# Kernel optimization log

Hardware: AMD Instinct MI355X
Metric: run time of the kernel (lower is better)

The kernel has to match this reference:

```python
import jax, jax.numpy as jnp
import numpy as np

N = 8192
K = 64

def setup_inputs() -> dict:
    key = jax.random.key(0)
    kw, ky = jax.random.split(key)
    W = jax.random.uniform(kw, (N, N), dtype=jnp.float32)
    Y = jax.random.normal(ky, (N, K), dtype=jnp.float32)
    return {"W": W, "Y": Y}

def reference(W, Y):
    # SpectralNetLoss(normalized=False):
    #   Dy[i,j] = ||y_i - y_j||^2 ; loss = sum(W * Dy) / (2n)
    n = Y.shape[0]
    sq = jnp.sum(Y * Y, axis=1)                      # (n,)
    # squared pairwise distances: ||y_i||^2 + ||y_j||^2 - 2 y_i.y_j
    Dy = sq[:, None] + sq[None, :] - 2.0 * (Y @ Y.T)  # (n, n)
    Dy = jnp.maximum(Dy, 0.0)  # clamp tiny negatives from cancellation (cdist is nonneg)
    loss = jnp.sum(W * Dy) / (2.0 * n)
    return loss
```

## Files before the change

### kernel.cpp

```cpp
#include <hip/hip_runtime.h>
#include <stdint.h>

#define N 8192
#define K 64
#define TILE 128
#define JT 8
#define NSTEP (4 * JT)

typedef __attribute__((ext_vector_type(8))) short bf16x8;
typedef __attribute__((ext_vector_type(4))) float floatx4;
typedef __attribute__((ext_vector_type(4))) unsigned short ushort4v;

__global__ __launch_bounds__(256) void prep_kernel(const float* __restrict__ Y,
                                                   unsigned short* __restrict__ Ybf,
                                                   float* __restrict__ sq,
                                                   float* __restrict__ out) {
    if (blockIdx.x == 0 && threadIdx.x == 0) out[0] = 0.0f;
    const int t = blockIdx.x * 256 + threadIdx.x;
    floatx4 v = *reinterpret_cast<const floatx4*>(Y + (size_t)t * 4);
    ushort4v o;
    #pragma unroll
    for (int e = 0; e < 4; ++e) {
        uint32_t bits = __float_as_uint(v[e]);
        uint32_t rnd  = bits + 0x7FFF + ((bits >> 16) & 1);
        o[e] = (unsigned short)(rnd >> 16);
    }
    *reinterpret_cast<ushort4v*>(Ybf + (size_t)t * 4) = o;
    float s = v[0]*v[0] + v[1]*v[1] + v[2]*v[2] + v[3]*v[3];
    #pragma unroll
    for (int m = 8; m >= 1; m >>= 1) s += __shfl_xor(s, m, 64);
    if ((threadIdx.x & 15) == 0) sq[t >> 4] = s;
}

__global__ __launch_bounds__(256, 2) void loss_kernel(const float* __restrict__ W,
                                                      const unsigned short* __restrict__ Ybf,
                                                      const float* __restrict__ sq,
                                                      float* __restrict__ out) {
    __shared__ float wsum[4];

    const int i0   = (blockIdx.x >> 3) * TILE;
    const int j0   = (blockIdx.x & 7) * (TILE * JT);
    const int tid  = threadIdx.x;
    const int wv   = tid >> 6;
    const int lane = tid & 63;
    const int qRow = (wv >> 1) * 64;
    const int qCol = (wv & 1) * 64;
    const int laneM = lane & 15;
    const int kq    = lane >> 4;

    bf16x8 afrag[2][4];
    float  sqi[4];
    #pragma unroll
    for (int mt = 0; mt < 4; ++mt) {
        const int row = i0 + qRow + mt * 16 + laneM;
        afrag[0][mt] = *reinterpret_cast<const bf16x8*>(Ybf + (size_t)row * K + kq * 8);
        afrag[1][mt] = *reinterpret_cast<const bf16x8*>(Ybf + (size_t)row * K + 32 + kq * 8);
        sqi[mt] = sq[row];
    }

    bf16x8  bfr[2][2][4];
    floatx4 sqjb[2][4];
    #pragma unroll
    for (int nt = 0; nt < 4; ++nt) {
        const int row = j0 + qCol + nt * 16 + laneM;
        bfr[0][0][nt] = *reinterpret_cast<const bf16x8*>(Ybf + (size_t)row * K + kq * 8);
        bfr[0][1][nt] = *reinterpret_cast<const bf16x8*>(Ybf + (size_t)row * K + 32 + kq * 8);
        sqjb[0][nt]   = *reinterpret_cast<const floatx4*>(sq + j0 + qCol + nt * 16 + kq * 4);
    }

    const float* wl = W + (size_t)(i0 + qRow + laneM) * N + (j0 + qCol + kq * 4);

    floatx4 wfb[4][4];
    #pragma unroll
    for (int g = 0; g < 4; ++g)
        #pragma unroll
        for (int nt = 0; nt < 4; ++nt)
            wfb[g][nt] = *reinterpret_cast<const floatx4*>(wl + (size_t)g * 16 * N + nt * 16);

    float p0 = 0.f, p1 = 0.f, p2 = 0.f, p3 = 0.f;

    #pragma unroll
    for (int s = 0; s < NSTEP; ++s) {
        const int mt  = s & 3;
        const int jt  = s >> 2;
        const int buf = jt & 1;

        if (mt == 0 && jt + 1 < JT) {
            #pragma unroll
            for (int nt = 0; nt < 4; ++nt) {
                const int row = j0 + (jt + 1) * TILE + qCol + nt * 16 + laneM;
                bfr[buf ^ 1][0][nt] = *reinterpret_cast<const bf16x8*>(Ybf + (size_t)row * K + kq * 8);
                bfr[buf ^ 1][1][nt] = *reinterpret_cast<const bf16x8*>(Ybf + (size_t)row * K + 32 + kq * 8);
                sqjb[buf ^ 1][nt]   = *reinterpret_cast<const floatx4*>(sq + j0 + (jt + 1) * TILE + qCol + nt * 16 + kq * 4);
            }
        }

        floatx4 accv[4];
        #pragma unroll
        for (int nt = 0; nt < 4; ++nt) accv[nt] = (floatx4){0.f, 0.f, 0.f, 0.f};
        #pragma unroll
        for (int ks = 0; ks < 2; ++ks)
            #pragma unroll
            for (int nt = 0; nt < 4; ++nt)
                accv[nt] = __builtin_amdgcn_mfma_f32_16x16x32_bf16(bfr[buf][ks][nt], afrag[ks][mt], accv[nt], 0, 0, 0);

        const float si = sqi[mt];
        #pragma unroll
        for (int nt = 0; nt < 4; ++nt) {
            const floatx4 g  = accv[nt];
            const floatx4 w4 = wfb[s & 3][nt];
            const floatx4 sj = sqjb[buf][nt];
            p0 = fmaf(w4[0], fmaxf(si + sj[0] - 2.0f * g[0], 0.f), p0);
            p1 = fmaf(w4[1], fmaxf(si + sj[1] - 2.0f * g[1], 0.f), p1);
            p2 = fmaf(w4[2], fmaxf(si + sj[2] - 2.0f * g[2], 0.f), p2);
            p3 = fmaf(w4[3], fmaxf(si + sj[3] - 2.0f * g[3], 0.f), p3);
        }

        if (s + 4 < NSTEP) {
            #pragma unroll
            for (int nt = 0; nt < 4; ++nt)
                wfb[s & 3][nt] = *reinterpret_cast<const floatx4*>(
                    wl + (size_t)mt * 16 * N + (jt + 1) * TILE + nt * 16);
        }
    }

    float partial = (p0 + p1) + (p2 + p3);
    #pragma unroll
    for (int m = 32; m >= 1; m >>= 1) partial += __shfl_xor(partial, m, 64);
    if (lane == 0) wsum[wv] = partial;
    __syncthreads();
    if (tid == 0) {
        float tot = (wsum[0] + wsum[1]) + (wsum[2] + wsum[3]);
        atomicAdd(out, tot * (1.0f / (2.0f * (float)N)));
    }
}

extern "C" void kernel_launch(void* const* d_in, const int* in_sizes, int n_in,
                              void* d_out, int out_size, void* d_ws, size_t ws_size,
                              hipStream_t stream) {
    const float* W = (const float*)d_in[0];
    const float* Y = (const float*)d_in[1];
    float* out = (float*)d_out;

    unsigned short* Ybf = (unsigned short*)d_ws;
    float* sq = (float*)((char*)d_ws + (size_t)N * K * 2);

    prep_kernel<<<(N * K / 4) / 256, 256, 0, stream>>>(Y, Ybf, sq, out);
    loss_kernel<<<(N / TILE) * (N / (TILE * JT)), 256, 0, stream>>>(W, Ybf, sq, out);
}
```

Before: 376.8 us.

## Shrink per-wave tiles and quadruple grid for higher occupancy

Reorganizes the loss kernel so each wave handles 32 rows by 256 columns instead of a 64x64 quadrant swept over 8 tiles. The grid grows from 512 to 2048 blocks, with launch bounds raised to 4 blocks per CU. W is double-buffered per 32-column step, and B fragments are loaded directly each iteration. The aim is more memory-level parallelism and lower register pressure for streaming W, at the cost of a shallower per-wave prefetch and repeated Y fragment loads.

```diff
diff --git a/kernel.cpp b/kernel.cpp
--- a/kernel.cpp
+++ b/kernel.cpp
@@ -3,9 +3,7 @@
 
 #define N 8192
 #define K 64
-#define TILE 128
-#define JT 8
-#define NSTEP (4 * JT)
+#define JT_PER 8
 
 typedef __attribute__((ext_vector_type(8))) short bf16x8;
 typedef __attribute__((ext_vector_type(4))) float floatx4;
@@ -32,95 +30,93 @@
     if ((threadIdx.x & 15) == 0) sq[t >> 4] = s;
 }
 
-__global__ __launch_bounds__(256, 2) void loss_kernel(const float* __restrict__ W,
+__global__ __launch_bounds__(256, 4) void loss_kernel(const float* __restrict__ W,
                                                       const unsigned short* __restrict__ Ybf,
                                                       const float* __restrict__ sq,
                                                       float* __restrict__ out) {
     __shared__ float wsum[4];
 
-    const int i0   = (blockIdx.x >> 3) * TILE;
-    const int j0   = (blockIdx.x & 7) * (TILE * JT);
+    const int bid  = blockIdx.x;
+    const int i0   = (bid >> 5) * 128;
+    const int j0   = (bid & 31) * 256;
     const int tid  = threadIdx.x;
     const int wv   = tid >> 6;
     const int lane = tid & 63;
-    const int qRow = (wv >> 1) * 64;
-    const int qCol = (wv & 1) * 64;
     const int laneM = lane & 15;
     const int kq    = lane >> 4;
+    const int iw    = i0 + wv * 32;
 
-    bf16x8 afrag[2][4];
-    float  sqi[4];
+    bf16x8 a[2][2];
+    float  sqi[2];
     #pragma unroll
-    for (int mt = 0; mt < 4; ++mt) {
-        const int row = i0 + qRow + mt * 16 + laneM;
-        afrag[0][mt] = *reinterpret_cast<const bf16x8*>(Ybf + (size_t)row * K + kq * 8);
-        afrag[1][mt] = *reinterpret_cast<const bf16x8*>(Ybf + (size_t)row * K + 32 + kq * 8);
-        sqi[mt] = sq[row];
+    for (int mt = 0; mt < 2; ++mt) {
+        const int row = iw + mt * 16 + laneM;
+        a[mt][0] = *reinterpret_cast<const bf16x8*>(Ybf + (size_t)row * K + kq * 8);
+        a[mt][1] = *reinterpret_cast<const bf16x8*>(Ybf + (size_t)row * K + 32 + kq * 8);
+        sqi[mt]  = sq[row];
     }
 
-    bf16x8  bfr[2][2][4];
-    floatx4 sqjb[2][4];
+    const float* wp0 = W + (size_t)(iw + laneM) * N + j0 + kq * 4;
+    const float* wp1 = wp0 + (size_t)16 * N;
+
+    floatx4 wbuf[2][2][2];
     #pragma unroll
-    for (int nt = 0; nt < 4; ++nt) {
-        const int row = j0 + qCol + nt * 16 + laneM;
-        bfr[0][0][nt] = *reinterpret_cast<const bf16x8*>(Ybf + (size_t)row * K + kq * 8);
-        bfr[0][1][nt] = *reinterpret_cast<const bf16x8*>(Ybf + (size_t)row * K + 32 + kq * 8);
-        sqjb[0][nt]   = *reinterpret_cast<const floatx4*>(sq + j0 + qCol + nt * 16 + kq * 4);
+    for (int nt = 0; nt < 2; ++nt) {
+        wbuf[0][0][nt] = *reinterpret_cast<const floatx4*>(wp0 + nt * 16);
+        wbuf[0][1][nt] = *reinterpret_cast<const floatx4*>(wp1 + nt * 16);
     }
-
-    const float* wl = W + (size_t)(i0 + qRow + laneM) * N + (j0 + qCol + kq * 4);
-
-    floatx4 wfb[4][4];
-    #pragma unroll
-    for (int g = 0; g < 4; ++g)
-        #pragma unroll
-        for (int nt = 0; nt < 4; ++nt)
-            wfb[g][nt] = *reinterpret_cast<const floatx4*>(wl + (size_t)g * 16 * N + nt * 16);
 
     float p0 = 0.f, p1 = 0.f, p2 = 0.f, p3 = 0.f;
 
     #pragma unroll
-    for (int s = 0; s < NSTEP; ++s) {
-        const int mt  = s & 3;
-        const int jt  = s >> 2;
-        const int buf = jt & 1;
+    for (int jt = 0; jt < JT_PER; ++jt) {
+        const int pp = jt & 1;
+        const int jb = j0 + jt * 32;
 
-        if (mt == 0 && jt + 1 < JT) {
+        bf16x8  b[2][2];
+        floatx4 sjq[2];
+        #pragma unroll
+        for (int nt = 0; nt < 2; ++nt) {
+            const int rowj = jb + nt * 16 + laneM;
+            b[nt][0] = *reinterpret_cast<const bf16x8*>(Ybf + (size_t)rowj * K + kq * 8);
+            b[nt][1] = *reinterpret_cast<const bf16x8*>(Ybf + (size_t)rowj * K + 32 + kq * 8);
+            sjq[nt]  = *reinterpret_cast<const floatx4*>(sq + jb + nt * 16 + kq * 4);
+        }
+
+        if (jt + 1 < JT_PER) {
             #pragma unroll
-            for (int nt = 0; nt < 4; ++nt) {
-                const int row = j0 + (jt + 1) * TILE + qCol + nt * 16 + laneM;
-                bfr[buf ^ 1][0][nt] = *reinterpret_cast<const bf16x8*>(Ybf + (size_t)row * K + kq * 8);
-                bfr[buf ^ 1][1][nt] = *reinterpret_cast<const bf16x8*>(Ybf + (size_t)row * K + 32 + kq * 8);
-                sqjb[buf ^ 1][nt]   = *reinterpret_cast<const floatx4*>(sq + j0 + (jt + 1) * TILE + qCol + nt * 16 + kq * 4);
+            for (int nt = 0; nt < 2; ++nt) {
+                wbuf[pp ^ 1][0][nt] = *reinterpret_cast<const floatx4*>(wp0 + (jt + 1) * 32 + nt * 16);
+                wbuf[pp ^ 1][1][nt] = *reinterpret_cast<const floatx4*>(wp1 + (jt + 1) * 32 + nt * 16);
             }
         }
 
-        floatx4 accv[4];
+        floatx4 acc[2][2];
         #pragma unroll
-        for (int nt = 0; nt < 4; ++nt) accv[nt] = (floatx4){0.f, 0.f, 0.f, 0.f};
+        for (int mt = 0; mt < 2; ++mt)
+            #pragma unroll
+            for (int nt = 0; nt < 2; ++nt) acc[mt][nt] = (floatx4){0.f, 0.f, 0.f, 0.f};
         #pragma unroll
         for (int ks = 0; ks < 2; ++ks)
             #pragma unroll
-            for (int nt = 0; nt < 4; ++nt)
-                accv[nt] = __builtin_amdgcn_mfma_f32_16x16x32_bf16(bfr[buf][ks][nt], afrag[ks][mt], accv[nt], 0, 0, 0);
+            for (int mt = 0; mt < 2; ++mt)
+                #pragma unroll
+                for (int nt = 0; nt < 2; ++nt)
+                    acc[mt][nt] = __builtin_amdgcn_mfma_f32_16x16x32_bf16(b[nt][ks], a[mt][ks], acc[mt][nt], 0, 0, 0);
 
-        const float si = sqi[mt];
         #pragma unroll
-        for (int nt = 0; nt < 4; ++nt) {
-            const floatx4 g  = accv[nt];
-            const floatx4 w4 = wfb[s & 3][nt];
-            const floatx4 sj = sqjb[buf][nt];
-            p0 = fmaf(w4[0], fmaxf(si + sj[0] - 2.0f * g[0], 0.f), p0);
-            p1 = fmaf(w4[1], fmaxf(si + sj[1] - 2.0f * g[1], 0.f), p1);
-            p2 = fmaf(w4[2], fmaxf(si + sj[2] - 2.0f * g[2], 0.f), p2);
-            p3 = fmaf(w4[3], fmaxf(si + sj[3] - 2.0f * g[3], 0.f), p3);
-        }
-
-        if (s + 4 < NSTEP) {
+        for (int mt = 0; mt < 2; ++mt) {
+            const float si = sqi[mt];
             #pragma unroll
-            for (int nt = 0; nt < 4; ++nt)
-                wfb[s & 3][nt] = *reinterpret_cast<const floatx4*>(
-                    wl + (size_t)mt * 16 * N + (jt + 1) * TILE + nt * 16);
+            for (int nt = 0; nt < 2; ++nt) {
+                const floatx4 g  = acc[mt][nt];
+                const floatx4 w4 = wbuf[pp][mt][nt];
+                const floatx4 sj = sjq[nt];
+                p0 = fmaf(w4[0], fmaxf(si + sj[0] - 2.0f * g[0], 0.f), p0);
+                p1 = fmaf(w4[1], fmaxf(si + sj[1] - 2.0f * g[1], 0.f), p1);
+                p2 = fmaf(w4[2], fmaxf(si + sj[2] - 2.0f * g[2], 0.f), p2);
+                p3 = fmaf(w4[3], fmaxf(si + sj[3] - 2.0f * g[3], 0.f), p3);
+            }
         }
     }
 
@@ -146,5 +142,5 @@
     float* sq = (float*)((char*)d_ws + (size_t)N * K * 2);
 
     prep_kernel<<<(N * K / 4) / 256, 256, 0, stream>>>(Y, Ybf, sq, out);
-    loss_kernel<<<(N / TILE) * (N / (TILE * JT)), 256, 0, stream>>>(W, Ybf, sq, out);
+    loss_kernel<<<64 * 32, 256, 0, stream>>>(W, Ybf, sq, out);
 }
```

Result: faster. 365.3 us (-3.1%).
